# Kernel optimization log

Hardware: AMD Instinct MI355X
Metric: run time of the kernel (lower is better)

The kernel has to match this reference:

```python
import jax, jax.numpy as jnp
import numpy as np

NUM_LAYERS = 2
FEATURES = 128
INPUT_SIZE = 128
HIDDEN = 512
BATCH = 128
SEQ_LEN = 512
PRED_LEN = 128


def _uniform(key, shape, fan):
    bound = 1.0 / np.sqrt(fan)
    return jax.random.uniform(key, shape, jnp.float32, -bound, bound)


def setup_inputs() -> dict:
    key = jax.random.key(0)
    ks = jax.random.split(key, 14)
    inp = {}
    inp["x"] = jax.random.normal(ks[0], (BATCH, SEQ_LEN, FEATURES), jnp.float32)
    # encoder Linear(features -> input_size)
    inp["enc_w"] = _uniform(ks[1], (INPUT_SIZE, FEATURES), FEATURES)
    inp["enc_b"] = _uniform(ks[2], (INPUT_SIZE,), FEATURES)
    # decoder Linear(hidden -> input_size)
    inp["dec_w"] = _uniform(ks[3], (INPUT_SIZE, HIDDEN), HIDDEN)
    inp["dec_b"] = _uniform(ks[4], (INPUT_SIZE,), HIDDEN)
    # LSTM layer 0 (input_size -> hidden), gate order i,f,g,o as in PyTorch
    inp["wih0"] = _uniform(ks[5], (4 * HIDDEN, INPUT_SIZE), HIDDEN)
    inp["whh0"] = _uniform(ks[6], (4 * HIDDEN, HIDDEN), HIDDEN)
    inp["bih0"] = _uniform(ks[7], (4 * HIDDEN,), HIDDEN)
    inp["bhh0"] = _uniform(ks[8], (4 * HIDDEN,), HIDDEN)
    # LSTM layer 1 (hidden -> hidden)
    inp["wih1"] = _uniform(ks[9], (4 * HIDDEN, HIDDEN), HIDDEN)
    inp["whh1"] = _uniform(ks[10], (4 * HIDDEN, HIDDEN), HIDDEN)
    inp["bih1"] = _uniform(ks[11], (4 * HIDDEN,), HIDDEN)
    inp["bhh1"] = _uniform(ks[12], (4 * HIDDEN,), HIDDEN)
    inp["pred_len"] = PRED_LEN
    return inp


def _lstm_cell(h, c, inp, wih, whh, bih, bhh):
    g = inp @ wih.T + bih + h @ whh.T + bhh  # [B, 4H]
    i, f, gg, o = jnp.split(g, 4, axis=-1)
    c = jax.nn.sigmoid(f) * c + jax.nn.sigmoid(i) * jnp.tanh(gg)
    h = jax.nn.sigmoid(o) * jnp.tanh(c)
    return h, c


def reference(x, enc_w, enc_b, dec_w, dec_b, wih0, whh0, bih0, bhh0,
              wih1, whh1, bih1, bhh1, pred_len):
    B, S, Fdim = x.shape
    T = S + pred_len - 1
    # pad x to T steps; beyond S the input comes from the previous output
    x_pad = jnp.concatenate([x, jnp.zeros((B, pred_len - 1, Fdim), x.dtype)], axis=1)
    x_t = jnp.transpose(x_pad, (1, 0, 2))  # [T, B, F]

    def step(carry, xs):
        h0, c0, h1, c1, prev_out = carry
        xt, t = xs
        inp = jnp.where(t < S, xt, prev_out)
        e = inp @ enc_w.T + enc_b                    # encoder
        h0, c0 = _lstm_cell(h0, c0, e, wih0, whh0, bih0, bhh0)
        h1, c1 = _lstm_cell(h1, c1, h0, wih1, whh1, bih1, bhh1)
        out = h1 @ dec_w.T + dec_b                   # decoder
        return (h0, c0, h1, c1, out), out

    z = jnp.zeros((B, HIDDEN), x.dtype)
    init = (z, z, z, z, jnp.zeros((B, Fdim), x.dtype))
    _, outs = jax.lax.scan(step, init, (x_t, jnp.arange(T)))
    # keep steps idx >= S-1 (pred_len outputs), back to [B, pred_len, input_size]
    return jnp.transpose(outs[S - 1:], (1, 0, 2))
```

## Files before the change

### kernel.cpp

```cpp
#include <hip/hip_runtime.h>
#include <math.h>

#define BATCH 128
#define HID 512
#define FEAT 128
#define SEQL 512
#define PREDL 128
#define LDSP 17

__device__ __forceinline__ float sigf_(float x) {
  return 1.0f / (1.0f + __expf(-x));
}
__device__ __forceinline__ float tanh_(float x) {
  float ax = fabsf(x);
  float e2 = __expf(-2.0f * ax);
  float t = (1.0f - e2) / (1.0f + e2);
  return copysignf(t, x);
}

template <bool HAS_B3>
__device__ __forceinline__ void cell_core(
    int wg,
    const float* __restrict__ A, const float* __restrict__ WA,
    const float* __restrict__ Hin, const float* __restrict__ WH,
    const float* __restrict__ b1, const float* __restrict__ b2,
    const float* __restrict__ b3,
    float* __restrict__ C, float* __restrict__ Hout,
    float* __restrict__ a_s, float* __restrict__ h_s) {
  const int tid = threadIdx.x;
  const int ut = (wg & 7) * 4 + ((wg >> 3) & 3);
  const int bt = wg >> 5;
  const int b0 = bt * 16;

  for (int idx = tid; idx < 16 * HID; idx += 256) {
    const int k = idx & (HID - 1);
    const int bb = idx >> 9;
    a_s[k * LDSP + bb] = A[(size_t)(b0 + bb) * HID + k];
    h_s[k * LDSP + bb] = Hin[(size_t)(b0 + bb) * HID + k];
  }
  __syncthreads();

  const int u = tid >> 4, b = tid & 15;
  const int ug = ut * 16 + u;

  float acc0 = b1[ug] + b2[ug];
  float acc1 = b1[512 + ug] + b2[512 + ug];
  float acc2 = b1[1024 + ug] + b2[1024 + ug];
  float acc3 = b1[1536 + ug] + b2[1536 + ug];
  if (HAS_B3) {
    acc0 += b3[ug]; acc1 += b3[512 + ug];
    acc2 += b3[1024 + ug]; acc3 += b3[1536 + ug];
  }

  const float4* __restrict__ wa0 = (const float4*)(WA + (size_t)ug * HID);
  const float4* __restrict__ wa1 = (const float4*)(WA + (size_t)(512 + ug) * HID);
  const float4* __restrict__ wa2 = (const float4*)(WA + (size_t)(1024 + ug) * HID);
  const float4* __restrict__ wa3 = (const float4*)(WA + (size_t)(1536 + ug) * HID);
  const float4* __restrict__ wh0 = (const float4*)(WH + (size_t)ug * HID);
  const float4* __restrict__ wh1 = (const float4*)(WH + (size_t)(512 + ug) * HID);
  const float4* __restrict__ wh2 = (const float4*)(WH + (size_t)(1024 + ug) * HID);
  const float4* __restrict__ wh3 = (const float4*)(WH + (size_t)(1536 + ug) * HID);

#pragma unroll 2
  for (int k4 = 0; k4 < HID / 4; ++k4) {
    const int k = k4 * 4;
    const float a0 = a_s[k * LDSP + b];
    const float a1 = a_s[(k + 1) * LDSP + b];
    const float a2 = a_s[(k + 2) * LDSP + b];
    const float a3 = a_s[(k + 3) * LDSP + b];
    const float h0 = h_s[k * LDSP + b];
    const float h1 = h_s[(k + 1) * LDSP + b];
    const float h2 = h_s[(k + 2) * LDSP + b];
    const float h3 = h_s[(k + 3) * LDSP + b];
    float4 w;
    w = wa0[k4]; acc0 += w.x * a0 + w.y * a1 + w.z * a2 + w.w * a3;
    w = wa1[k4]; acc1 += w.x * a0 + w.y * a1 + w.z * a2 + w.w * a3;
    w = wa2[k4]; acc2 += w.x * a0 + w.y * a1 + w.z * a2 + w.w * a3;
    w = wa3[k4]; acc3 += w.x * a0 + w.y * a1 + w.z * a2 + w.w * a3;
    w = wh0[k4]; acc0 += w.x * h0 + w.y * h1 + w.z * h2 + w.w * h3;
    w = wh1[k4]; acc1 += w.x * h0 + w.y * h1 + w.z * h2 + w.w * h3;
    w = wh2[k4]; acc2 += w.x * h0 + w.y * h1 + w.z * h2 + w.w * h3;
    w = wh3[k4]; acc3 += w.x * h0 + w.y * h1 + w.z * h2 + w.w * h3;
  }

  const size_t ci = (size_t)(b0 + b) * HID + ug;
  const float ig = sigf_(acc0), fg = sigf_(acc1);
  const float gg = tanh_(acc2), og = sigf_(acc3);
  const float cn = fg * C[ci] + ig * gg;
  C[ci] = cn;
  Hout[ci] = og * tanh_(cn);
}

__device__ __forceinline__ void step0_core(
    int wg, const float* __restrict__ x, int t,
    const float* __restrict__ enc_w, const float* __restrict__ enc_b,
    const float* __restrict__ wih0, const float* __restrict__ whh0,
    const float* __restrict__ bih0, const float* __restrict__ bhh0,
    const float* __restrict__ Hin, float* __restrict__ C,
    float* __restrict__ Hout,
    float* __restrict__ xe_s, float* __restrict__ h_s) {
  const int tid = threadIdx.x;
  const int ut = (wg & 7) * 4 + ((wg >> 3) & 3);
  const int bt = wg >> 5;
  const int b0 = bt * 16;
  float* x_s = xe_s;
  float* e_s = xe_s + FEAT * LDSP;

  for (int idx = tid; idx < 16 * HID; idx += 256) {
    const int k = idx & (HID - 1);
    const int bb = idx >> 9;
    h_s[k * LDSP + bb] = Hin[(size_t)(b0 + bb) * HID + k];
  }
  for (int idx = tid; idx < 16 * FEAT; idx += 256) {
    const int k = idx & (FEAT - 1);
    const int bb = idx >> 7;
    x_s[k * LDSP + bb] = x[((size_t)(b0 + bb) * SEQL + t) * FEAT + k];
  }
  __syncthreads();

  {
    const int b = tid & 15, jg = tid >> 4;
#pragma unroll
    for (int jj = 0; jj < 8; ++jj) {
      const int j = jg * 8 + jj;
      float acc = enc_b[j];
      const float4* __restrict__ wr = (const float4*)(enc_w + (size_t)j * FEAT);
#pragma unroll 4
      for (int k4 = 0; k4 < FEAT / 4; ++k4) {
        const float4 w = wr[k4];
        const int k = k4 * 4;
        acc += w.x * x_s[k * LDSP + b] + w.y * x_s[(k + 1) * LDSP + b] +
               w.z * x_s[(k + 2) * LDSP + b] + w.w * x_s[(k + 3) * LDSP + b];
      }
      e_s[j * LDSP + b] = acc;
    }
  }
  __syncthreads();

  const int u = tid >> 4, b = tid & 15;
  const int ug = ut * 16 + u;
  float acc0 = bih0[ug] + bhh0[ug];
  float acc1 = bih0[512 + ug] + bhh0[512 + ug];
  float acc2 = bih0[1024 + ug] + bhh0[1024 + ug];
  float acc3 = bih0[1536 + ug] + bhh0[1536 + ug];

  const float4* __restrict__ wh0 = (const float4*)(whh0 + (size_t)ug * HID);
  const float4* __restrict__ wh1 = (const float4*)(whh0 + (size_t)(512 + ug) * HID);
  const float4* __restrict__ wh2 = (const float4*)(whh0 + (size_t)(1024 + ug) * HID);
  const float4* __restrict__ wh3 = (const float4*)(whh0 + (size_t)(1536 + ug) * HID);
#pragma unroll 2
  for (int k4 = 0; k4 < HID / 4; ++k4) {
    const int k = k4 * 4;
    const float h0 = h_s[k * LDSP + b];
    const float h1 = h_s[(k + 1) * LDSP + b];
    const float h2 = h_s[(k + 2) * LDSP + b];
    const float h3 = h_s[(k + 3) * LDSP + b];
    float4 w;
    w = wh0[k4]; acc0 += w.x * h0 + w.y * h1 + w.z * h2 + w.w * h3;
    w = wh1[k4]; acc1 += w.x * h0 + w.y * h1 + w.z * h2 + w.w * h3;
    w = wh2[k4]; acc2 += w.x * h0 + w.y * h1 + w.z * h2 + w.w * h3;
    w = wh3[k4]; acc3 += w.x * h0 + w.y * h1 + w.z * h2 + w.w * h3;
  }
  const float4* __restrict__ wi0 = (const float4*)(wih0 + (size_t)ug * FEAT);
  const float4* __restrict__ wi1 = (const float4*)(wih0 + (size_t)(512 + ug) * FEAT);
  const float4* __restrict__ wi2 = (const float4*)(wih0 + (size_t)(1024 + ug) * FEAT);
  const float4* __restrict__ wi3 = (const float4*)(wih0 + (size_t)(1536 + ug) * FEAT);
#pragma unroll 2
  for (int k4 = 0; k4 < FEAT / 4; ++k4) {
    const int k = k4 * 4;
    const float e0 = e_s[k * LDSP + b];
    const float e1 = e_s[(k + 1) * LDSP + b];
    const float e2 = e_s[(k + 2) * LDSP + b];
    const float e3 = e_s[(k + 3) * LDSP + b];
    float4 w;
    w = wi0[k4]; acc0 += w.x * e0 + w.y * e1 + w.z * e2 + w.w * e3;
    w = wi1[k4]; acc1 += w.x * e0 + w.y * e1 + w.z * e2 + w.w * e3;
    w = wi2[k4]; acc2 += w.x * e0 + w.y * e1 + w.z * e2 + w.w * e3;
    w = wi3[k4]; acc3 += w.x * e0 + w.y * e1 + w.z * e2 + w.w * e3;
  }

  const size_t ci = (size_t)(b0 + b) * HID + ug;
  const float ig = sigf_(acc0), fg = sigf_(acc1);
  const float gg = tanh_(acc2), og = sigf_(acc3);
  const float cn = fg * C[ci] + ig * gg;
  C[ci] = cn;
  Hout[ci] = og * tanh_(cn);
}

__device__ __forceinline__ void dec_core(
    int wg, const float* __restrict__ h1, const float* __restrict__ dec_w,
    const float* __restrict__ dec_b, float* __restrict__ out, int step,
    float* __restrict__ h_s) {
  const int tid = threadIdx.x;
  const int jt = wg & 7, bt = wg >> 3, b0 = bt * 16;
  for (int idx = tid; idx < 16 * HID; idx += 256) {
    const int k = idx & (HID - 1);
    const int bb = idx >> 9;
    h_s[k * LDSP + bb] = h1[(size_t)(b0 + bb) * HID + k];
  }
  __syncthreads();
  const int jl = tid & 15, b = tid >> 4;
  const int j = jt * 16 + jl;
  float acc = dec_b[j];
  const float4* __restrict__ wr = (const float4*)(dec_w + (size_t)j * HID);
#pragma unroll 2
  for (int k4 = 0; k4 < HID / 4; ++k4) {
    const float4 w = wr[k4];
    const int k = k4 * 4;
    acc += w.x * h_s[k * LDSP + b] + w.y * h_s[(k + 1) * LDSP + b] +
           w.z * h_s[(k + 2) * LDSP + b] + w.w * h_s[(k + 3) * LDSP + b];
  }
  out[((size_t)(b0 + b) * PREDL + step) * FEAT + j] = acc;
}


__global__ __launch_bounds__(256, 2) void k_tick_tf(
    const float* __restrict__ x,
    const float* __restrict__ enc_w, const float* __restrict__ enc_b,
    const float* __restrict__ wih0, const float* __restrict__ whh0,
    const float* __restrict__ bih0, const float* __restrict__ bhh0,
    const float* __restrict__ wih1, const float* __restrict__ whh1,
    const float* __restrict__ bih1, const float* __restrict__ bhh1,
    const float* __restrict__ h0in, float* __restrict__ c0,
    float* __restrict__ h0out,
    const float* __restrict__ h1in, float* __restrict__ c1,
    float* __restrict__ h1out, int t) {
  __shared__ float s1[HID * LDSP];
  __shared__ float s2[HID * LDSP];
  const int wg = blockIdx.x;
  if (wg < 256) {
    step0_core(wg, x, t, enc_w, enc_b, wih0, whh0, bih0, bhh0,
               h0in, c0, h0out, s1, s2);
  } else if (t > 0) {
    cell_core<false>(wg - 256, h0in, wih1, h1in, whh1, bih1, bhh1, nullptr,
                     c1, h1out, s1, s2);
  }
}

__global__ __launch_bounds__(256, 2) void k_cell(
    const float* __restrict__ A, const float* __restrict__ WA,
    const float* __restrict__ Hin, const float* __restrict__ WH,
    const float* __restrict__ b1, const float* __restrict__ b2,
    float* __restrict__ C, float* __restrict__ Hout) {
  __shared__ float s1[HID * LDSP];
  __shared__ float s2[HID * LDSP];
  cell_core<false>(blockIdx.x, A, WA, Hin, WH, b1, b2, nullptr, C, Hout, s1, s2);
}

__global__ __launch_bounds__(256, 2) void k_ar_a(
    const float* __restrict__ h1prev, const float* __restrict__ Wcomp,
    const float* __restrict__ h0in, const float* __restrict__ whh0,
    const float* __restrict__ bih0, const float* __restrict__ bhh0,
    const float* __restrict__ bcomp, float* __restrict__ c0,
    float* __restrict__ h0out,
    const float* __restrict__ dec_w, const float* __restrict__ dec_b,
    float* __restrict__ out, int step) {
  __shared__ float s1[HID * LDSP];
  __shared__ float s2[HID * LDSP];
  const int wg = blockIdx.x;
  if (wg < 256) {
    cell_core<true>(wg, h1prev, Wcomp, h0in, whh0, bih0, bhh0, bcomp,
                    c0, h0out, s1, s2);
  } else {
    dec_core(wg - 256, h1prev, dec_w, dec_b, out, step, s2);
  }
}

__global__ __launch_bounds__(256, 2) void k_dec(
    const float* __restrict__ h1, const float* __restrict__ dec_w,
    const float* __restrict__ dec_b, float* __restrict__ out, int step) {
  __shared__ float s2[HID * LDSP];
  dec_core(blockIdx.x, h1, dec_w, dec_b, out, step, s2);
}

__global__ void k_b1(const float* __restrict__ enc_w,
                     const float* __restrict__ dec_w, float* __restrict__ B1) {
  const int idx = blockIdx.x * 256 + threadIdx.x;
  const int j = idx >> 9, m = idx & 511;
  float acc = 0.0f;
  for (int k = 0; k < FEAT; ++k) acc += enc_w[j * FEAT + k] * dec_w[k * HID + m];
  B1[idx] = acc;
}
__global__ void k_wcomp(const float* __restrict__ wih0,
                        const float* __restrict__ B1, float* __restrict__ W) {
  const size_t idx = (size_t)blockIdx.x * 256 + threadIdx.x;
  const int n = (int)(idx >> 9), m = (int)(idx & 511);
  float acc = 0.0f;
  for (int k = 0; k < FEAT; ++k) acc += wih0[n * FEAT + k] * B1[k * HID + m];
  W[idx] = acc;
}
__global__ void k_te(const float* __restrict__ enc_w,
                     const float* __restrict__ enc_b,
                     const float* __restrict__ dec_b, float* __restrict__ te) {
  const int j = threadIdx.x;
  float acc = enc_b[j];
  for (int k = 0; k < FEAT; ++k) acc += dec_b[k] * enc_w[j * FEAT + k];
  te[j] = acc;
}
__global__ void k_bcomp(const float* __restrict__ wih0,
                        const float* __restrict__ te, float* __restrict__ bc) {
  const int n = blockIdx.x * 256 + threadIdx.x;
  float acc = 0.0f;
  for (int j = 0; j < FEAT; ++j) acc += wih0[n * FEAT + j] * te[j];
  bc[n] = acc;
}

extern "C" void kernel_launch(void* const* d_in, const int* in_sizes, int n_in,
                              void* d_out, int out_size, void* d_ws,
                              size_t ws_size, hipStream_t stream) {
  const float* x     = (const float*)d_in[0];
  const float* enc_w = (const float*)d_in[1];
  const float* enc_b = (const float*)d_in[2];
  const float* dec_w = (const float*)d_in[3];
  const float* dec_b = (const float*)d_in[4];
  const float* wih0  = (const float*)d_in[5];
  const float* whh0  = (const float*)d_in[6];
  const float* bih0  = (const float*)d_in[7];
  const float* bhh0  = (const float*)d_in[8];
  const float* wih1  = (const float*)d_in[9];
  const float* whh1  = (const float*)d_in[10];
  const float* bih1  = (const float*)d_in[11];
  const float* bhh1  = (const float*)d_in[12];
  float* out = (float*)d_out;

  float* ws = (float*)d_ws;
  float* Wcomp = ws;
  float* B1    = ws + 1048576;
  float* te    = ws + 1114112;
  float* bcomp = ws + 1114240;
  float* h0b0  = ws + 1116288;
  float* h0b[2] = { h0b0, h0b0 + 65536 };
  float* h1b[2] = { h0b0 + 2 * 65536, h0b0 + 3 * 65536 };
  float* c0 = h0b0 + 4 * 65536;
  float* c1 = h0b0 + 5 * 65536;

  hipMemsetAsync(h0b0, 0, (size_t)6 * 65536 * sizeof(float), stream);

  k_b1<<<256, 256, 0, stream>>>(enc_w, dec_w, B1);
  k_wcomp<<<4096, 256, 0, stream>>>(wih0, B1, Wcomp);
  k_te<<<1, 128, 0, stream>>>(enc_w, enc_b, dec_b, te);
  k_bcomp<<<8, 256, 0, stream>>>(wih0, te, bcomp);

  for (int t = 0; t < SEQL; ++t) {
    k_tick_tf<<<512, 256, 0, stream>>>(
        x, enc_w, enc_b, wih0, whh0, bih0, bhh0, wih1, whh1, bih1, bhh1,
        h0b[(t + 1) & 1], c0, h0b[t & 1],
        h1b[t & 1], c1, h1b[(t + 1) & 1], t);
  }
  k_cell<<<256, 256, 0, stream>>>(h0b[1], wih1, h1b[0], whh1, bih1, bhh1,
                                  c1, h1b[1]);

  for (int t = SEQL; t < SEQL + PREDL - 1; ++t) {
    k_ar_a<<<320, 256, 0, stream>>>(
        h1b[(t + 1) & 1], Wcomp, h0b[(t + 1) & 1], whh0, bih0, bhh0, bcomp,
        c0, h0b[t & 1], dec_w, dec_b, out, t - SEQL);
    k_cell<<<256, 256, 0, stream>>>(h0b[t & 1], wih1, h1b[(t + 1) & 1], whh1,
                                    bih1, bhh1, c1, h1b[t & 1]);
  }
  k_dec<<<64, 256, 0, stream>>>(h1b[0], dec_w, dec_b, out, PREDL - 1);
}
```

Before: 39.94 ms.

## Replace per-step kernel launches with one persistent kernel using grid barriers

Replaces roughly 770 per-timestep kernel launches with a single persistent kernel of 256 workgroups, each with 512 threads. The two thread halves handle layer 0 and layer 1 of the LSTM, and steps are separated by a hierarchical atomic grid barrier. Cell state now stays in registers across steps instead of being read from and written to global memory. This removes launch overhead and C-state traffic. The cost is that correctness depends on all 256 workgroups being co-resident, plus spin-barrier latency and 512-thread blocks at 2 blocks per CU.

After: 63.33 ms. 1.59x slower.

```diff
diff --git a/kernel.cpp b/kernel.cpp
--- a/kernel.cpp
+++ b/kernel.cpp
@@ -1,276 +1,304 @@
 #include <hip/hip_runtime.h>
 #include <math.h>
 
-#define BATCH 128
 #define HID 512
 #define FEAT 128
 #define SEQL 512
 #define PREDL 128
 #define LDSP 17
-
-__device__ __forceinline__ float sigf_(float x) {
-  return 1.0f / (1.0f + __expf(-x));
-}
+#define NWG 256
+
+__device__ __forceinline__ float sigf_(float x) { return 1.0f / (1.0f + __expf(-x)); }
 __device__ __forceinline__ float tanh_(float x) {
   float ax = fabsf(x);
   float e2 = __expf(-2.0f * ax);
-  float t = (1.0f - e2) / (1.0f + e2);
-  return copysignf(t, x);
-}
-
-template <bool HAS_B3>
-__device__ __forceinline__ void cell_core(
-    int wg,
-    const float* __restrict__ A, const float* __restrict__ WA,
-    const float* __restrict__ Hin, const float* __restrict__ WH,
-    const float* __restrict__ b1, const float* __restrict__ b2,
-    const float* __restrict__ b3,
-    float* __restrict__ C, float* __restrict__ Hout,
-    float* __restrict__ a_s, float* __restrict__ h_s) {
-  const int tid = threadIdx.x;
-  const int ut = (wg & 7) * 4 + ((wg >> 3) & 3);
-  const int bt = wg >> 5;
-  const int b0 = bt * 16;
-
-  for (int idx = tid; idx < 16 * HID; idx += 256) {
+  return copysignf((1.0f - e2) / (1.0f + e2), x);
+}
+
+__device__ __forceinline__ float ldg_sc(const float* p) {
+  return __hip_atomic_load(p, __ATOMIC_RELAXED, __HIP_MEMORY_SCOPE_AGENT);
+}
+__device__ __forceinline__ void stg_sc(float* p, float v) {
+  __hip_atomic_store(p, v, __ATOMIC_RELAXED, __HIP_MEMORY_SCOPE_AGENT);
+}
+
+__device__ __forceinline__ void grid_bar(int* bar, int wg, int phase) {
+  __syncthreads();
+  if (threadIdx.x == 0) {
+    int* cxt = bar + (wg & 7) * 32;
+    const int a = __hip_atomic_fetch_add(cxt, 1, __ATOMIC_ACQ_REL, __HIP_MEMORY_SCOPE_AGENT);
+    if (a == 32 * phase - 1) {
+      const int r = __hip_atomic_fetch_add(bar + 8 * 32, 1, __ATOMIC_ACQ_REL, __HIP_MEMORY_SCOPE_AGENT);
+      if (r == 8 * phase - 1)
+        __hip_atomic_store(bar + 9 * 32, phase, __ATOMIC_RELEASE, __HIP_MEMORY_SCOPE_AGENT);
+    }
+    while (__hip_atomic_load(bar + 9 * 32, __ATOMIC_ACQUIRE, __HIP_MEMORY_SCOPE_AGENT) < phase)
+      __builtin_amdgcn_s_sleep(1);
+  }
+  __syncthreads();
+}
+
+__device__ __forceinline__ void stage_tile512(float* dst, const float* src,
+                                              int b0, int tid) {
+#pragma unroll
+  for (int idx = tid; idx < 16 * HID; idx += 512) {
     const int k = idx & (HID - 1);
     const int bb = idx >> 9;
-    a_s[k * LDSP + bb] = A[(size_t)(b0 + bb) * HID + k];
-    h_s[k * LDSP + bb] = Hin[(size_t)(b0 + bb) * HID + k];
-  }
-  __syncthreads();
-
-  const int u = tid >> 4, b = tid & 15;
-  const int ug = ut * 16 + u;
-
-  float acc0 = b1[ug] + b2[ug];
-  float acc1 = b1[512 + ug] + b2[512 + ug];
-  float acc2 = b1[1024 + ug] + b2[1024 + ug];
-  float acc3 = b1[1536 + ug] + b2[1536 + ug];
-  if (HAS_B3) {
-    acc0 += b3[ug]; acc1 += b3[512 + ug];
-    acc2 += b3[1024 + ug]; acc3 += b3[1536 + ug];
-  }
-
-  const float4* __restrict__ wa0 = (const float4*)(WA + (size_t)ug * HID);
-  const float4* __restrict__ wa1 = (const float4*)(WA + (size_t)(512 + ug) * HID);
-  const float4* __restrict__ wa2 = (const float4*)(WA + (size_t)(1024 + ug) * HID);
-  const float4* __restrict__ wa3 = (const float4*)(WA + (size_t)(1536 + ug) * HID);
-  const float4* __restrict__ wh0 = (const float4*)(WH + (size_t)ug * HID);
-  const float4* __restrict__ wh1 = (const float4*)(WH + (size_t)(512 + ug) * HID);
-  const float4* __restrict__ wh2 = (const float4*)(WH + (size_t)(1024 + ug) * HID);
-  const float4* __restrict__ wh3 = (const float4*)(WH + (size_t)(1536 + ug) * HID);
-
+    dst[k * LDSP + bb] = ldg_sc(src + (size_t)(b0 + bb) * HID + k);
+  }
+}
+__device__ __forceinline__ void stage_x(float* dst, const float* x, int t,
+                                        int b0, int tid) {
+#pragma unroll
+  for (int idx = tid; idx < 16 * FEAT; idx += 512) {
+    const int k = idx & (FEAT - 1);
+    const int bb = idx >> 7;
+    dst[k * LDSP + bb] = x[((size_t)(b0 + bb) * SEQL + t) * FEAT + k];
+  }
+}
+
+__device__ __forceinline__ void act_store(float acc0, float acc1, float acc2,
+                                          float acc3, float& c_reg,
+                                          float* Hout, size_t ci) {
+  const float ig = sigf_(acc0), fg = sigf_(acc1);
+  const float gg = tanh_(acc2), og = sigf_(acc3);
+  const float cn = fg * c_reg + ig * gg;
+  c_reg = cn;
+  stg_sc(Hout + ci, og * tanh_(cn));
+}
+
+__device__ __forceinline__ void cell512(
+    const float* __restrict__ sA,
+    const float4* __restrict__ a0, const float4* __restrict__ a1,
+    const float4* __restrict__ a2, const float4* __restrict__ a3,
+    const float* __restrict__ sH,
+    const float4* __restrict__ h0p, const float4* __restrict__ h1p,
+    const float4* __restrict__ h2p, const float4* __restrict__ h3p,
+    float i0, float i1, float i2, float i3,
+    int b, float& c_reg, float* __restrict__ Hout, size_t ci) {
+  float acc0 = i0, acc1 = i1, acc2 = i2, acc3 = i3;
 #pragma unroll 2
   for (int k4 = 0; k4 < HID / 4; ++k4) {
     const int k = k4 * 4;
-    const float a0 = a_s[k * LDSP + b];
-    const float a1 = a_s[(k + 1) * LDSP + b];
-    const float a2 = a_s[(k + 2) * LDSP + b];
-    const float a3 = a_s[(k + 3) * LDSP + b];
-    const float h0 = h_s[k * LDSP + b];
-    const float h1 = h_s[(k + 1) * LDSP + b];
-    const float h2 = h_s[(k + 2) * LDSP + b];
-    const float h3 = h_s[(k + 3) * LDSP + b];
+    const float A0 = sA[k * LDSP + b], A1 = sA[(k + 1) * LDSP + b];
+    const float A2 = sA[(k + 2) * LDSP + b], A3 = sA[(k + 3) * LDSP + b];
+    const float H0 = sH[k * LDSP + b], H1 = sH[(k + 1) * LDSP + b];
+    const float H2 = sH[(k + 2) * LDSP + b], H3 = sH[(k + 3) * LDSP + b];
     float4 w;
-    w = wa0[k4]; acc0 += w.x * a0 + w.y * a1 + w.z * a2 + w.w * a3;
-    w = wa1[k4]; acc1 += w.x * a0 + w.y * a1 + w.z * a2 + w.w * a3;
-    w = wa2[k4]; acc2 += w.x * a0 + w.y * a1 + w.z * a2 + w.w * a3;
-    w = wa3[k4]; acc3 += w.x * a0 + w.y * a1 + w.z * a2 + w.w * a3;
-    w = wh0[k4]; acc0 += w.x * h0 + w.y * h1 + w.z * h2 + w.w * h3;
-    w = wh1[k4]; acc1 += w.x * h0 + w.y * h1 + w.z * h2 + w.w * h3;
-    w = wh2[k4]; acc2 += w.x * h0 + w.y * h1 + w.z * h2 + w.w * h3;
-    w = wh3[k4]; acc3 += w.x * h0 + w.y * h1 + w.z * h2 + w.w * h3;
-  }
-
-  const size_t ci = (size_t)(b0 + b) * HID + ug;
-  const float ig = sigf_(acc0), fg = sigf_(acc1);
-  const float gg = tanh_(acc2), og = sigf_(acc3);
-  const float cn = fg * C[ci] + ig * gg;
-  C[ci] = cn;
-  Hout[ci] = og * tanh_(cn);
-}
-
-__device__ __forceinline__ void step0_core(
-    int wg, const float* __restrict__ x, int t,
-    const float* __restrict__ enc_w, const float* __restrict__ enc_b,
-    const float* __restrict__ wih0, const float* __restrict__ whh0,
-    const float* __restrict__ bih0, const float* __restrict__ bhh0,
-    const float* __restrict__ Hin, float* __restrict__ C,
-    float* __restrict__ Hout,
-    float* __restrict__ xe_s, float* __restrict__ h_s) {
-  const int tid = threadIdx.x;
-  const int ut = (wg & 7) * 4 + ((wg >> 3) & 3);
-  const int bt = wg >> 5;
-  const int b0 = bt * 16;
-  float* x_s = xe_s;
-  float* e_s = xe_s + FEAT * LDSP;
-
-  for (int idx = tid; idx < 16 * HID; idx += 256) {
-    const int k = idx & (HID - 1);
-    const int bb = idx >> 9;
-    h_s[k * LDSP + bb] = Hin[(size_t)(b0 + bb) * HID + k];
-  }
-  for (int idx = tid; idx < 16 * FEAT; idx += 256) {
-    const int k = idx & (FEAT - 1);
-    const int bb = idx >> 7;
-    x_s[k * LDSP + bb] = x[((size_t)(b0 + bb) * SEQL + t) * FEAT + k];
-  }
-  __syncthreads();
-
-  {
-    const int b = tid & 15, jg = tid >> 4;
-#pragma unroll
-    for (int jj = 0; jj < 8; ++jj) {
-      const int j = jg * 8 + jj;
-      float acc = enc_b[j];
-      const float4* __restrict__ wr = (const float4*)(enc_w + (size_t)j * FEAT);
-#pragma unroll 4
-      for (int k4 = 0; k4 < FEAT / 4; ++k4) {
-        const float4 w = wr[k4];
-        const int k = k4 * 4;
-        acc += w.x * x_s[k * LDSP + b] + w.y * x_s[(k + 1) * LDSP + b] +
-               w.z * x_s[(k + 2) * LDSP + b] + w.w * x_s[(k + 3) * LDSP + b];
-      }
-      e_s[j * LDSP + b] = acc;
-    }
-  }
-  __syncthreads();
-
-  const int u = tid >> 4, b = tid & 15;
-  const int ug = ut * 16 + u;
-  float acc0 = bih0[ug] + bhh0[ug];
-  float acc1 = bih0[512 + ug] + bhh0[512 + ug];
-  float acc2 = bih0[1024 + ug] + bhh0[1024 + ug];
-  float acc3 = bih0[1536 + ug] + bhh0[1536 + ug];
-
-  const float4* __restrict__ wh0 = (const float4*)(whh0 + (size_t)ug * HID);
-  const float4* __restrict__ wh1 = (const float4*)(whh0 + (size_t)(512 + ug) * HID);
-  const float4* __restrict__ wh2 = (const float4*)(whh0 + (size_t)(1024 + ug) * HID);
-  const float4* __restrict__ wh3 = (const float4*)(whh0 + (size_t)(1536 + ug) * HID);
+    w = a0[k4];  acc0 += w.x * A0 + w.y * A1 + w.z * A2 + w.w * A3;
+    w = a1[k4];  acc1 += w.x * A0 + w.y * A1 + w.z * A2 + w.w * A3;
+    w = a2[k4];  acc2 += w.x * A0 + w.y * A1 + w.z * A2 + w.w * A3;
+    w = a3[k4];  acc3 += w.x * A0 + w.y * A1 + w.z * A2 + w.w * A3;
+    w = h0p[k4]; acc0 += w.x * H0 + w.y * H1 + w.z * H2 + w.w * H3;
+    w = h1p[k4]; acc1 += w.x * H0 + w.y * H1 + w.z * H2 + w.w * H3;
+    w = h2p[k4]; acc2 += w.x * H0 + w.y * H1 + w.z * H2 + w.w * H3;
+    w = h3p[k4]; acc3 += w.x * H0 + w.y * H1 + w.z * H2 + w.w * H3;
+  }
+  act_store(acc0, acc1, acc2, acc3, c_reg, Hout, ci);
+}
+
+__device__ __forceinline__ void cell0tf(
+    const float* __restrict__ sE, const float* __restrict__ sH,
+    const float4* __restrict__ e0, const float4* __restrict__ e1,
+    const float4* __restrict__ e2, const float4* __restrict__ e3,
+    const float4* __restrict__ h0p, const float4* __restrict__ h1p,
+    const float4* __restrict__ h2p, const float4* __restrict__ h3p,
+    float i0, float i1, float i2, float i3,
+    int b, float& c_reg, float* __restrict__ Hout, size_t ci) {
+  float acc0 = i0, acc1 = i1, acc2 = i2, acc3 = i3;
 #pragma unroll 2
   for (int k4 = 0; k4 < HID / 4; ++k4) {
     const int k = k4 * 4;
-    const float h0 = h_s[k * LDSP + b];
-    const float h1 = h_s[(k + 1) * LDSP + b];
-    const float h2 = h_s[(k + 2) * LDSP + b];
-    const float h3 = h_s[(k + 3) * LDSP + b];
+    const float H0 = sH[k * LDSP + b], H1 = sH[(k + 1) * LDSP + b];
+    const float H2 = sH[(k + 2) * LDSP + b], H3 = sH[(k + 3) * LDSP + b];
     float4 w;
-    w = wh0[k4]; acc0 += w.x * h0 + w.y * h1 + w.z * h2 + w.w * h3;
-    w = wh1[k4]; acc1 += w.x * h0 + w.y * h1 + w.z * h2 + w.w * h3;
-    w = wh2[k4]; acc2 += w.x * h0 + w.y * h1 + w.z * h2 + w.w * h3;
-    w = wh3[k4]; acc3 += w.x * h0 + w.y * h1 + w.z * h2 + w.w * h3;
-  }
-  const float4* __restrict__ wi0 = (const float4*)(wih0 + (size_t)ug * FEAT);
-  const float4* __restrict__ wi1 = (const float4*)(wih0 + (size_t)(512 + ug) * FEAT);
-  const float4* __restrict__ wi2 = (const float4*)(wih0 + (size_t)(1024 + ug) * FEAT);
-  const float4* __restrict__ wi3 = (const float4*)(wih0 + (size_t)(1536 + ug) * FEAT);
+    w = h0p[k4]; acc0 += w.x * H0 + w.y * H1 + w.z * H2 + w.w * H3;
+    w = h1p[k4]; acc1 += w.x * H0 + w.y * H1 + w.z * H2 + w.w * H3;
+    w = h2p[k4]; acc2 += w.x * H0 + w.y * H1 + w.z * H2 + w.w * H3;
+    w = h3p[k4]; acc3 += w.x * H0 + w.y * H1 + w.z * H2 + w.w * H3;
+  }
 #pragma unroll 2
   for (int k4 = 0; k4 < FEAT / 4; ++k4) {
     const int k = k4 * 4;
-    const float e0 = e_s[k * LDSP + b];
-    const float e1 = e_s[(k + 1) * LDSP + b];
-    const float e2 = e_s[(k + 2) * LDSP + b];
-    const float e3 = e_s[(k + 3) * LDSP + b];
+    const float E0 = sE[k * LDSP + b], E1 = sE[(k + 1) * LDSP + b];
+    const float E2 = sE[(k + 2) * LDSP + b], E3 = sE[(k + 3) * LDSP + b];
     float4 w;
-    w = wi0[k4]; acc0 += w.x * e0 + w.y * e1 + w.z * e2 + w.w * e3;
-    w = wi1[k4]; acc1 += w.x * e0 + w.y * e1 + w.z * e2 + w.w * e3;
-    w = wi2[k4]; acc2 += w.x * e0 + w.y * e1 + w.z * e2 + w.w * e3;
-    w = wi3[k4]; acc3 += w.x * e0 + w.y * e1 + w.z * e2 + w.w * e3;
-  }
-
-  const size_t ci = (size_t)(b0 + b) * HID + ug;
-  const float ig = sigf_(acc0), fg = sigf_(acc1);
-  const float gg = tanh_(acc2), og = sigf_(acc3);
-  const float cn = fg * C[ci] + ig * gg;
-  C[ci] = cn;
-  Hout[ci] = og * tanh_(cn);
-}
-
-__device__ __forceinline__ void dec_core(
-    int wg, const float* __restrict__ h1, const float* __restrict__ dec_w,
-    const float* __restrict__ dec_b, float* __restrict__ out, int step,
-    float* __restrict__ h_s) {
-  const int tid = threadIdx.x;
-  const int jt = wg & 7, bt = wg >> 3, b0 = bt * 16;
-  for (int idx = tid; idx < 16 * HID; idx += 256) {
-    const int k = idx & (HID - 1);
-    const int bb = idx >> 9;
-    h_s[k * LDSP + bb] = h1[(size_t)(b0 + bb) * HID + k];
-  }
-  __syncthreads();
-  const int jl = tid & 15, b = tid >> 4;
-  const int j = jt * 16 + jl;
-  float acc = dec_b[j];
-  const float4* __restrict__ wr = (const float4*)(dec_w + (size_t)j * HID);
+    w = e0[k4]; acc0 += w.x * E0 + w.y * E1 + w.z * E2 + w.w * E3;
+    w = e1[k4]; acc1 += w.x * E0 + w.y * E1 + w.z * E2 + w.w * E3;
+    w = e2[k4]; acc2 += w.x * E0 + w.y * E1 + w.z * E2 + w.w * E3;
+    w = e3[k4]; acc3 += w.x * E0 + w.y * E1 + w.z * E2 + w.w * E3;
+  }
+  act_store(acc0, acc1, acc2, acc3, c_reg, Hout, ci);
+}
+
+__device__ __forceinline__ void dec_body(const float* __restrict__ sH1,
+                                         const float4* __restrict__ decr,
+                                         float decb, int b0, int bd, int jdec,
+                                         float* __restrict__ out, int step) {
+  float acc = decb;
 #pragma unroll 2
   for (int k4 = 0; k4 < HID / 4; ++k4) {
-    const float4 w = wr[k4];
     const int k = k4 * 4;
-    acc += w.x * h_s[k * LDSP + b] + w.y * h_s[(k + 1) * LDSP + b] +
-           w.z * h_s[(k + 2) * LDSP + b] + w.w * h_s[(k + 3) * LDSP + b];
-  }
-  out[((size_t)(b0 + b) * PREDL + step) * FEAT + j] = acc;
-}
-
-
-__global__ __launch_bounds__(256, 2) void k_tick_tf(
+    const float4 w = decr[k4];
+    acc += w.x * sH1[k * LDSP + bd] + w.y * sH1[(k + 1) * LDSP + bd] +
+           w.z * sH1[(k + 2) * LDSP + bd] + w.w * sH1[(k + 3) * LDSP + bd];
+  }
+  out[((size_t)(b0 + bd) * PREDL + step) * FEAT + jdec] = acc;
+}
+
+__global__ __launch_bounds__(512, 2) void k_persist(
     const float* __restrict__ x,
     const float* __restrict__ enc_w, const float* __restrict__ enc_b,
     const float* __restrict__ wih0, const float* __restrict__ whh0,
     const float* __restrict__ bih0, const float* __restrict__ bhh0,
     const float* __restrict__ wih1, const float* __restrict__ whh1,
     const float* __restrict__ bih1, const float* __restrict__ bhh1,
-    const float* __restrict__ h0in, float* __restrict__ c0,
-    float* __restrict__ h0out,
-    const float* __restrict__ h1in, float* __restrict__ c1,
-    float* __restrict__ h1out, int t) {
-  __shared__ float s1[HID * LDSP];
-  __shared__ float s2[HID * LDSP];
+    const float* __restrict__ dec_w, const float* __restrict__ dec_b,
+    const float* __restrict__ Wcomp, const float* __restrict__ bcomp,
+    float* __restrict__ h0A, float* __restrict__ h0B,
+    float* __restrict__ h1A, float* __restrict__ h1B,
+    int* __restrict__ bar, float* __restrict__ out) {
+  __shared__ float s_h0[HID * LDSP];
+  __shared__ float s_h1[HID * LDSP];
+  __shared__ float s_x[FEAT * LDSP];
+  __shared__ float s_e[FEAT * LDSP];
+
   const int wg = blockIdx.x;
-  if (wg < 256) {
-    step0_core(wg, x, t, enc_w, enc_b, wih0, whh0, bih0, bhh0,
-               h0in, c0, h0out, s1, s2);
-  } else if (t > 0) {
-    cell_core<false>(wg - 256, h0in, wih1, h1in, whh1, bih1, bhh1, nullptr,
-                     c1, h1out, s1, s2);
-  }
-}
-
-__global__ __launch_bounds__(256, 2) void k_cell(
-    const float* __restrict__ A, const float* __restrict__ WA,
-    const float* __restrict__ Hin, const float* __restrict__ WH,
-    const float* __restrict__ b1, const float* __restrict__ b2,
-    float* __restrict__ C, float* __restrict__ Hout) {
-  __shared__ float s1[HID * LDSP];
-  __shared__ float s2[HID * LDSP];
-  cell_core<false>(blockIdx.x, A, WA, Hin, WH, b1, b2, nullptr, C, Hout, s1, s2);
-}
-
-__global__ __launch_bounds__(256, 2) void k_ar_a(
-    const float* __restrict__ h1prev, const float* __restrict__ Wcomp,
-    const float* __restrict__ h0in, const float* __restrict__ whh0,
-    const float* __restrict__ bih0, const float* __restrict__ bhh0,
-    const float* __restrict__ bcomp, float* __restrict__ c0,
-    float* __restrict__ h0out,
-    const float* __restrict__ dec_w, const float* __restrict__ dec_b,
-    float* __restrict__ out, int step) {
-  __shared__ float s1[HID * LDSP];
-  __shared__ float s2[HID * LDSP];
-  const int wg = blockIdx.x;
-  if (wg < 256) {
-    cell_core<true>(wg, h1prev, Wcomp, h0in, whh0, bih0, bhh0, bcomp,
-                    c0, h0out, s1, s2);
-  } else {
-    dec_core(wg - 256, h1prev, dec_w, dec_b, out, step, s2);
-  }
-}
-
-__global__ __launch_bounds__(256, 2) void k_dec(
-    const float* __restrict__ h1, const float* __restrict__ dec_w,
-    const float* __restrict__ dec_b, float* __restrict__ out, int step) {
-  __shared__ float s2[HID * LDSP];
-  dec_core(blockIdx.x, h1, dec_w, dec_b, out, step, s2);
+  const int tid = threadIdx.x;
+  const int ut = (wg & 7) * 4 + ((wg >> 3) & 3);
+  const int bt = wg >> 5;
+  const int b0 = bt * 16;
+  const int half = tid >> 8;
+  const int t8 = tid & 255;
+  const int u = t8 >> 4, b = t8 & 15;
+  const int ug = ut * 16 + u;
+  const size_t ci = (size_t)(b0 + b) * HID + ug;
+
+  float* h0buf[2] = {h0A, h0B};
+  float* h1buf[2] = {h1A, h1B};
+
+  const float4* e0p = (const float4*)(wih0 + (size_t)ug * FEAT);
+  const float4* e1p = (const float4*)(wih0 + (size_t)(512 + ug) * FEAT);
+  const float4* e2p = (const float4*)(wih0 + (size_t)(1024 + ug) * FEAT);
+  const float4* e3p = (const float4*)(wih0 + (size_t)(1536 + ug) * FEAT);
+  const float4* H00 = (const float4*)(whh0 + (size_t)ug * HID);
+  const float4* H01 = (const float4*)(whh0 + (size_t)(512 + ug) * HID);
+  const float4* H02 = (const float4*)(whh0 + (size_t)(1024 + ug) * HID);
+  const float4* H03 = (const float4*)(whh0 + (size_t)(1536 + ug) * HID);
+  const float4* Wc0 = (const float4*)(Wcomp + (size_t)ug * HID);
+  const float4* Wc1 = (const float4*)(Wcomp + (size_t)(512 + ug) * HID);
+  const float4* Wc2 = (const float4*)(Wcomp + (size_t)(1024 + ug) * HID);
+  const float4* Wc3 = (const float4*)(Wcomp + (size_t)(1536 + ug) * HID);
+  const float4* I10 = (const float4*)(wih1 + (size_t)ug * HID);
+  const float4* I11 = (const float4*)(wih1 + (size_t)(512 + ug) * HID);
+  const float4* I12 = (const float4*)(wih1 + (size_t)(1024 + ug) * HID);
+  const float4* I13 = (const float4*)(wih1 + (size_t)(1536 + ug) * HID);
+  const float4* H10 = (const float4*)(whh1 + (size_t)ug * HID);
+  const float4* H11 = (const float4*)(whh1 + (size_t)(512 + ug) * HID);
+  const float4* H12 = (const float4*)(whh1 + (size_t)(1024 + ug) * HID);
+  const float4* H13 = (const float4*)(whh1 + (size_t)(1536 + ug) * HID);
+  const float bt00 = bih0[ug] + bhh0[ug];
+  const float bt01 = bih0[512 + ug] + bhh0[512 + ug];
+  const float bt02 = bih0[1024 + ug] + bhh0[1024 + ug];
+  const float bt03 = bih0[1536 + ug] + bhh0[1536 + ug];
+  const float ba00 = bt00 + bcomp[ug];
+  const float ba01 = bt01 + bcomp[512 + ug];
+  const float ba02 = bt02 + bcomp[1024 + ug];
+  const float ba03 = bt03 + bcomp[1536 + ug];
+  const float b10 = bih1[ug] + bhh1[ug];
+  const float b11 = bih1[512 + ug] + bhh1[512 + ug];
+  const float b12 = bih1[1024 + ug] + bhh1[1024 + ug];
+  const float b13 = bih1[1536 + ug] + bhh1[1536 + ug];
+
+  const int is_dec = (half == 1) && (((wg >> 3) & 3) == 0);
+  const int jdec = (wg & 7) * 16 + (t8 >> 4);
+  const int bd = t8 & 15;
+  const float4* decr = (const float4*)(dec_w + (size_t)jdec * HID);
+  const float decb = dec_b[jdec];
+
+  float c_reg = 0.0f;
+  int ph = 0;
+
+  for (int t = 0; t < SEQL; ++t) {
+    const float* h0in = h0buf[(t + 1) & 1];
+    float* h0out = h0buf[t & 1];
+    const float* h1in = h1buf[t & 1];
+    float* h1out = h1buf[(t + 1) & 1];
+
+    stage_tile512(s_h0, h0in, b0, tid);
+    stage_tile512(s_h1, h1in, b0, tid);
+    stage_x(s_x, x, t, b0, tid);
+    __syncthreads();
+
+    {
+      const int be = tid & 15, jg = tid >> 4;
+#pragma unroll
+      for (int jj = 0; jj < 4; ++jj) {
+        const int j = jg * 4 + jj;
+        float acc = enc_b[j];
+        const float4* wr = (const float4*)(enc_w + (size_t)j * FEAT);
+#pragma unroll 4
+        for (int k4 = 0; k4 < FEAT / 4; ++k4) {
+          const float4 w = wr[k4];
+          const int k = k4 * 4;
+          acc += w.x * s_x[k * LDSP + be] + w.y * s_x[(k + 1) * LDSP + be] +
+                 w.z * s_x[(k + 2) * LDSP + be] + w.w * s_x[(k + 3) * LDSP + be];
+        }
+        s_e[j * LDSP + be] = acc;
+      }
+    }
+    __syncthreads();
+
+    if (half == 0) {
+      cell0tf(s_e, s_h0, e0p, e1p, e2p, e3p, H00, H01, H02, H03,
+              bt00, bt01, bt02, bt03, b, c_reg, h0out, ci);
+    } else if (t > 0) {
+      cell512(s_h0, I10, I11, I12, I13, s_h1, H10, H11, H12, H13,
+              b10, b11, b12, b13, b, c_reg, h1out, ci);
+    }
+    grid_bar(bar, wg, ++ph);
+  }
+
+  stage_tile512(s_h0, h0buf[1], b0, tid);
+  stage_tile512(s_h1, h1buf[0], b0, tid);
+  __syncthreads();
+  if (half == 1) {
+    cell512(s_h0, I10, I11, I12, I13, s_h1, H10, H11, H12, H13,
+            b10, b11, b12, b13, b, c_reg, h1buf[1], ci);
+  }
+  grid_bar(bar, wg, ++ph);
+
+  for (int t = SEQL; t < SEQL + PREDL - 1; ++t) {
+    const float* h1prev = h1buf[(t + 1) & 1];
+    const float* h0prev = h0buf[(t + 1) & 1];
+    float* h0cur = h0buf[t & 1];
+    float* h1cur = h1buf[t & 1];
+
+    stage_tile512(s_h1, h1prev, b0, tid);
+    stage_tile512(s_h0, h0prev, b0, tid);
+    __syncthreads();
+    if (half == 0) {
+      cell512(s_h1, Wc0, Wc1, Wc2, Wc3, s_h0, H00, H01, H02, H03,
+              ba00, ba01, ba02, ba03, b, c_reg, h0cur, ci);
+    } else if (is_dec) {
+      dec_body(s_h1, decr, decb, b0, bd, jdec, out, t - SEQL);
+    }
+    grid_bar(bar, wg, ++ph);
+
+    stage_tile512(s_h0, h0cur, b0, tid);
+    __syncthreads();
+    if (half == 1) {
+      cell512(s_h0, I10, I11, I12, I13, s_h1, H10, H11, H12, H13,
+              b10, b11, b12, b13, b, c_reg, h1cur, ci);
+    }
+    grid_bar(bar, wg, ++ph);
+  }
+
+  stage_tile512(s_h1, h1buf[0], b0, tid);
+  __syncthreads();
+  if (is_dec) {
+    dec_body(s_h1, decr, decb, b0, bd, jdec, out, PREDL - 1);
+  }
 }
 
 __global__ void k_b1(const float* __restrict__ enc_w,
@@ -324,38 +352,23 @@
   float* out = (float*)d_out;
 
   float* ws = (float*)d_ws;
-  float* Wcomp = ws;
-  float* B1    = ws + 1048576;
-  float* te    = ws + 1114112;
-  float* bcomp = ws + 1114240;
-  float* h0b0  = ws + 1116288;
-  float* h0b[2] = { h0b0, h0b0 + 65536 };
-  float* h1b[2] = { h0b0 + 2 * 65536, h0b0 + 3 * 65536 };
-  float* c0 = h0b0 + 4 * 65536;
-  float* c1 = h0b0 + 5 * 65536;
-
-  hipMemsetAsync(h0b0, 0, (size_t)6 * 65536 * sizeof(float), stream);
+  float* h0b0  = ws;
+  float* h1b0  = ws + 131072;
+  int*   bar   = (int*)(ws + 262144);
+  float* Wcomp = ws + 263168;
+  float* B1    = ws + 1311744;
+  float* te    = ws + 1377280;
+  float* bcomp = ws + 1377408;
+
+  hipMemsetAsync(ws, 0, (size_t)263168 * sizeof(float), stream);
 
   k_b1<<<256, 256, 0, stream>>>(enc_w, dec_w, B1);
   k_wcomp<<<4096, 256, 0, stream>>>(wih0, B1, Wcomp);
   k_te<<<1, 128, 0, stream>>>(enc_w, enc_b, dec_b, te);
   k_bcomp<<<8, 256, 0, stream>>>(wih0, te, bcomp);
 
-  for (int t = 0; t < SEQL; ++t) {
-    k_tick_tf<<<512, 256, 0, stream>>>(
-        x, enc_w, enc_b, wih0, whh0, bih0, bhh0, wih1, whh1, bih1, bhh1,
-        h0b[(t + 1) & 1], c0, h0b[t & 1],
-        h1b[t & 1], c1, h1b[(t + 1) & 1], t);
-  }
-  k_cell<<<256, 256, 0, stream>>>(h0b[1], wih1, h1b[0], whh1, bih1, bhh1,
-                                  c1, h1b[1]);
-
-  for (int t = SEQL; t < SEQL + PREDL - 1; ++t) {
-    k_ar_a<<<320, 256, 0, stream>>>(
-        h1b[(t + 1) & 1], Wcomp, h0b[(t + 1) & 1], whh0, bih0, bhh0, bcomp,
-        c0, h0b[t & 1], dec_w, dec_b, out, t - SEQL);
-    k_cell<<<256, 256, 0, stream>>>(h0b[t & 1], wih1, h1b[(t + 1) & 1], whh1,
-                                    bih1, bhh1, c1, h1b[t & 1]);
-  }
-  k_dec<<<64, 256, 0, stream>>>(h1b[0], dec_w, dec_b, out, PREDL - 1);
-}
+  k_persist<<<NWG, 512, 0, stream>>>(
+      x, enc_w, enc_b, wih0, whh0, bih0, bhh0, wih1, whh1, bih1, bhh1,
+      dec_w, dec_b, Wcomp, bcomp,
+      h0b0, h0b0 + 65536, h1b0, h1b0 + 65536, bar, out);
+}
```
